# Kernel optimization log

Hardware: AMD Instinct MI355X
Metric: run time of the kernel (lower is better)

The kernel has to match this reference:

```python
import jax, jax.numpy as jnp
import numpy as np

STATE_LEN, SEQ_LEN, HIDDEN = 2048, 4096, 2048

def setup_inputs() -> dict:
    key = jax.random.key(0)
    k1, k2, k3, k4 = jax.random.split(key, 4)
    scale = 1.0 / np.sqrt(HIDDEN)
    return {
        "out_state": jax.random.normal(k1, (STATE_LEN, HIDDEN), dtype=jnp.float32),
        "history": jax.random.normal(k2, (SEQ_LEN, HIDDEN), dtype=jnp.float32),
        "W": jax.random.normal(k3, (HIDDEN, HIDDEN), dtype=jnp.float32) * scale,
        "b": jax.random.normal(k4, (HIDDEN,), dtype=jnp.float32) * scale,
    }

def reference(out_state, history, W, b):
    # method='general': energy_j = Linear(history_j) = history_j @ W.T + b
    # score[i, j] = out_state_i . energy_j  -> batched GEMM replacing the double loop
    energies = history @ W.T + b                 # [seq_len, hidden]
    scores = jnp.einsum('ih,jh->ij', out_state, energies)  # [state_len, seq_len]
    # F.softmax on a 2D tensor (legacy default) normalizes over dim=1 (rows)
    return jax.nn.softmax(scores, axis=-1)
```

## Files before the change

kernel.cpp:

```cpp
#include <hip/hip_runtime.h>


#define STATE_LEN 2048
#define SEQ_LEN   4096
#define HIDDEN    2048

#define BM 128
#define BK 32

typedef __bf16 bf16x8 __attribute__((ext_vector_type(8)));
typedef float f32x4 __attribute__((ext_vector_type(4)));

__device__ __forceinline__ unsigned short f32_to_bf16(float f) {
  unsigned u = __float_as_uint(f);
  u += 0x7FFFu + ((u >> 16) & 1u);
  return (unsigned short)(u >> 16);
}
__device__ __forceinline__ float bf16_to_f32(unsigned short h) {
  return __uint_as_float(((unsigned)h) << 16);
}

__device__ __forceinline__ void gld16(const void* g, void* l) {
  __builtin_amdgcn_global_load_lds(
      (const __attribute__((address_space(1))) unsigned int*)g,
      (__attribute__((address_space(3))) unsigned int*)l,
      16, 0, 0);
}

__global__ __launch_bounds__(256) void split_kernel(
    const float* __restrict__ in, unsigned short* __restrict__ hi,
    unsigned short* __restrict__ lo, int n) {
  int i = (blockIdx.x * 256 + threadIdx.x) * 4;
  if (i >= n) return;
  float4 v = *(const float4*)&in[i];
  ushort4 h, l;
  h.x = f32_to_bf16(v.x); l.x = f32_to_bf16(v.x - bf16_to_f32(h.x));
  h.y = f32_to_bf16(v.y); l.y = f32_to_bf16(v.y - bf16_to_f32(h.y));
  h.z = f32_to_bf16(v.z); l.z = f32_to_bf16(v.z - bf16_to_f32(h.z));
  h.w = f32_to_bf16(v.w); l.w = f32_to_bf16(v.w - bf16_to_f32(h.w));
  *(ushort4*)&hi[i] = h;
  *(ushort4*)&lo[i] = l;
}

__global__ __launch_bounds__(256) void transpose_split_kernel(
    const float* __restrict__ in, unsigned short* __restrict__ hi,
    unsigned short* __restrict__ lo, int rows, int cols) {
  __shared__ float tile[32][33];
  const int bx = blockIdx.x * 32;
  const int by = blockIdx.y * 32;
  const int tx = threadIdx.x;
  const int ty = threadIdx.y;
#pragma unroll
  for (int i = 0; i < 32; i += 8)
    tile[ty + i][tx] = in[(size_t)(by + ty + i) * cols + (bx + tx)];
  __syncthreads();
#pragma unroll
  for (int i = 0; i < 32; i += 8) {
    float x = tile[tx][ty + i];
    unsigned short h = f32_to_bf16(x);
    unsigned short l = f32_to_bf16(x - bf16_to_f32(h));
    size_t o = (size_t)(bx + ty + i) * rows + (by + tx);
    hi[o] = h;
    lo[o] = l;
  }
}

__global__ __launch_bounds__(256) void reduce_split4(
    const float* __restrict__ p0, const float* __restrict__ p1,
    const float* __restrict__ p2, const float* __restrict__ p3,
    unsigned short* __restrict__ hi, unsigned short* __restrict__ lo, int n) {
  int i = (blockIdx.x * 256 + threadIdx.x) * 4;
  if (i >= n) return;
  float4 a = *(const float4*)&p0[i];
  float4 b = *(const float4*)&p1[i];
  float4 c = *(const float4*)&p2[i];
  float4 d = *(const float4*)&p3[i];
  a.x = (a.x + b.x) + (c.x + d.x);
  a.y = (a.y + b.y) + (c.y + d.y);
  a.z = (a.z + b.z) + (c.z + d.z);
  a.w = (a.w + b.w) + (c.w + d.w);
  ushort4 h, l;
  h.x = f32_to_bf16(a.x); l.x = f32_to_bf16(a.x - bf16_to_f32(h.x));
  h.y = f32_to_bf16(a.y); l.y = f32_to_bf16(a.y - bf16_to_f32(h.y));
  h.z = f32_to_bf16(a.z); l.z = f32_to_bf16(a.z - bf16_to_f32(h.z));
  h.w = f32_to_bf16(a.w); l.w = f32_to_bf16(a.w - bf16_to_f32(h.w));
  *(ushort4*)&hi[i] = h;
  *(ushort4*)&lo[i] = l;
}

template <int BN, int KSPLIT>
__global__ __launch_bounds__(256, 4) void gemm_bt_split(
    const unsigned short* __restrict__ Ahi, const unsigned short* __restrict__ Alo,
    const unsigned short* __restrict__ Bhi, const unsigned short* __restrict__ Blo,
    float* __restrict__ Cf0, float* __restrict__ Cf1,
    float* __restrict__ Cf2, float* __restrict__ Cf3, int M, int N, int K) {
  constexpr int NI = BN / 32;
  __shared__ __align__(16) unsigned short sAhi[BM * BK];
  __shared__ __align__(16) unsigned short sAlo[BM * BK];
  __shared__ __align__(16) unsigned short sBhi[BN * BK];
  __shared__ __align__(16) unsigned short sBlo[BN * BK];

  const int t = threadIdx.x;
  const int tileM = blockIdx.y * BM;
  const int tileN = blockIdx.x * BN;
  const int z = (KSPLIT > 1) ? blockIdx.z : 0;
  const int kBase = z * (K / KSPLIT);
  const int kEnd = kBase + K / KSPLIT;
  float* Cf = Cf0;
  if (KSPLIT > 1) {
    if (z == 1) Cf = Cf1;
    else if (z == 2) Cf = Cf2;
    else if (z == 3) Cf = Cf3;
  }
  const int rr = t >> 2;
  const int cc = t & 3;

  const int lane = t & 63;
  const int wave = t >> 6;
  const int wm = wave >> 1;
  const int wn = wave & 1;
  const int lr = lane & 15;
  const int kqc = lane >> 4;

  f32x4 acc[4][NI] = {};

  for (int k0 = kBase; k0 < kEnd; k0 += BK) {
#pragma unroll
    for (int it = 0; it < 2; ++it) {
      const int r = it * 64 + rr;
      const int q = cc ^ ((r >> 1) & 3);
      const size_t ga = (size_t)(tileM + r) * K + k0 + q * 8;
      const int ls = r * BK + cc * 8;
      gld16(Ahi + ga, &sAhi[ls]);
      gld16(Alo + ga, &sAlo[ls]);
    }
#pragma unroll
    for (int it = 0; it < BN / 64; ++it) {
      const int r = it * 64 + rr;
      const int q = cc ^ ((r >> 1) & 3);
      const size_t gb = (size_t)(tileN + r) * K + k0 + q * 8;
      const int ls = r * BK + cc * 8;
      gld16(Bhi + gb, &sBhi[ls]);
      gld16(Blo + gb, &sBlo[ls]);
    }
    __syncthreads();

    bf16x8 ah[4], al[4], bh[NI], bl[NI];
#pragma unroll
    for (int mi = 0; mi < 4; ++mi) {
      const int R = wm * 64 + mi * 16 + lr;
      const int off = R * BK + (kqc ^ ((R >> 1) & 3)) * 8;
      ah[mi] = *(const bf16x8*)&sAhi[off];
      al[mi] = *(const bf16x8*)&sAlo[off];
    }
#pragma unroll
    for (int ni = 0; ni < NI; ++ni) {
      const int R = wn * (BN / 2) + ni * 16 + lr;
      const int off = R * BK + (kqc ^ ((R >> 1) & 3)) * 8;
      bh[ni] = *(const bf16x8*)&sBhi[off];
      bl[ni] = *(const bf16x8*)&sBlo[off];
    }
#pragma unroll
    for (int mi = 0; mi < 4; ++mi)
#pragma unroll
      for (int ni = 0; ni < NI; ++ni) {
        acc[mi][ni] = __builtin_amdgcn_mfma_f32_16x16x32_bf16(ah[mi], bh[ni], acc[mi][ni], 0, 0, 0);
        acc[mi][ni] = __builtin_amdgcn_mfma_f32_16x16x32_bf16(ah[mi], bl[ni], acc[mi][ni], 0, 0, 0);
        acc[mi][ni] = __builtin_amdgcn_mfma_f32_16x16x32_bf16(al[mi], bh[ni], acc[mi][ni], 0, 0, 0);
      }
    __syncthreads();
  }

#pragma unroll
  for (int mi = 0; mi < 4; ++mi)
#pragma unroll
    for (int ni = 0; ni < NI; ++ni)
#pragma unroll
      for (int e = 0; e < 4; ++e) {
        const int row = tileM + wm * 64 + mi * 16 + (lane >> 4) * 4 + e;
        const int col = tileN + wn * (BN / 2) + ni * 16 + lr;
        Cf[(size_t)row * N + col] = acc[mi][ni][e];
      }
}

__global__ __launch_bounds__(256) void reduce_softmax(float* __restrict__ d,
                                                      const float* __restrict__ part,
                                                      int cols) {
  const int row = blockIdx.x;
  float* p = d + (size_t)row * cols;
  const float* q = part + (size_t)row * cols;
  const int t = threadIdx.x;
  const int lane = t & 63;
  const int wave = t >> 6;
  __shared__ float sred[4];

  float4 v[4];
  float m = -3.0e38f;
#pragma unroll
  for (int k = 0; k < 4; ++k) {
    float4 a = *(const float4*)&p[(t + k * 256) * 4];
    float4 b = *(const float4*)&q[(t + k * 256) * 4];
    a.x += b.x; a.y += b.y; a.z += b.z; a.w += b.w;
    v[k] = a;
    m = fmaxf(m, fmaxf(fmaxf(a.x, a.y), fmaxf(a.z, a.w)));
  }
#pragma unroll
  for (int off = 32; off > 0; off >>= 1) m = fmaxf(m, __shfl_xor(m, off, 64));
  if (lane == 0) sred[wave] = m;
  __syncthreads();
  m = fmaxf(fmaxf(sred[0], sred[1]), fmaxf(sred[2], sred[3]));
  __syncthreads();

  float s = 0.f;
#pragma unroll
  for (int k = 0; k < 4; ++k) {
    v[k].x = __expf(v[k].x - m);
    v[k].y = __expf(v[k].y - m);
    v[k].z = __expf(v[k].z - m);
    v[k].w = __expf(v[k].w - m);
    s += (v[k].x + v[k].y) + (v[k].z + v[k].w);
  }
#pragma unroll
  for (int off = 32; off > 0; off >>= 1) s += __shfl_xor(s, off, 64);
  if (lane == 0) sred[wave] = s;
  __syncthreads();
  s = (sred[0] + sred[1]) + (sred[2] + sred[3]);
  const float inv = 1.0f / s;
#pragma unroll
  for (int k = 0; k < 4; ++k) {
    v[k].x *= inv; v[k].y *= inv; v[k].z *= inv; v[k].w *= inv;
    *(float4*)&p[(t + k * 256) * 4] = v[k];
  }
}

extern "C" void kernel_launch(void* const* d_in, const int* in_sizes, int n_in,
                              void* d_out, int out_size, void* d_ws, size_t ws_size,
                              hipStream_t stream) {
  const float* out_state = (const float*)d_in[0];
  const float* history   = (const float*)d_in[1];
  const float* W         = (const float*)d_in[2];
  float* out = (float*)d_out;

  char* ws = (char*)d_ws;
  const size_t MB = 1ull << 20;
  unsigned short* ohi  = (unsigned short*)(ws + 0 * MB);
  unsigned short* olo  = (unsigned short*)(ws + 8 * MB);
  unsigned short* wthi = (unsigned short*)(ws + 16 * MB);
  unsigned short* wtlo = (unsigned short*)(ws + 24 * MB);
  unsigned short* hhi  = (unsigned short*)(ws + 32 * MB);
  unsigned short* hlo  = (unsigned short*)(ws + 48 * MB);
  float*          pws  = (float*)(ws + 64 * MB);
  float* g1p0 = pws;
  float* g1p1 = pws + (size_t)STATE_LEN * HIDDEN;
  float* g1p2 = out;
  float* g1p3 = out + (size_t)STATE_LEN * HIDDEN;
  unsigned short* thi = (unsigned short*)(ws + 0 * MB);
  unsigned short* tlo = (unsigned short*)(ws + 8 * MB);

  split_kernel<<<(STATE_LEN * HIDDEN) / 1024, 256, 0, stream>>>(out_state, ohi, olo,
                                                                STATE_LEN * HIDDEN);
  transpose_split_kernel<<<dim3(HIDDEN / 32, HIDDEN / 32), dim3(32, 8), 0, stream>>>(
      W, wthi, wtlo, HIDDEN, HIDDEN);
  split_kernel<<<(SEQ_LEN * HIDDEN) / 1024, 256, 0, stream>>>(history, hhi, hlo,
                                                              SEQ_LEN * HIDDEN);
  gemm_bt_split<128, 4>
      <<<dim3(HIDDEN / 128, STATE_LEN / 128, 4), 256, 0, stream>>>(
          ohi, olo, wthi, wtlo, g1p0, g1p1, g1p2, g1p3, STATE_LEN, HIDDEN, HIDDEN);
  reduce_split4<<<(STATE_LEN * HIDDEN) / 1024, 256, 0, stream>>>(
      g1p0, g1p1, g1p2, g1p3, thi, tlo, STATE_LEN * HIDDEN);
  gemm_bt_split<128, 2>
      <<<dim3(SEQ_LEN / 128, STATE_LEN / 128, 2), 256, 0, stream>>>(
          thi, tlo, hhi, hlo, out, pws, nullptr, nullptr, STATE_LEN, SEQ_LEN, HIDDEN);
  reduce_softmax<<<STATE_LEN, 256, 0, stream>>>(out, pws, SEQ_LEN);
}
```

Before: 298.4 us.

## Load GEMM operands directly from global memory into registers, dropping LDS staging

The split-bf16 GEMM no longer stages A and B tiles through shared memory with global_load_lds and barriers. Each wave now reads its MFMA fragments straight from global memory into registers, which removes LDS traffic and the two __syncthreads per K step. The cost is that tile data is no longer shared between waves, so each operand fragment is fetched twice from global/L2. The 16-byte per-lane loads are also less coalesced, and launch bounds drop to 2 blocks per CU.

```diff
diff --git a/kernel.cpp b/kernel.cpp
--- a/kernel.cpp
+++ b/kernel.cpp
@@ -4,9 +4,6 @@
 #define STATE_LEN 2048
 #define SEQ_LEN   4096
 #define HIDDEN    2048
-
-#define BM 128
-#define BK 32
 
 typedef __bf16 bf16x8 __attribute__((ext_vector_type(8)));
 typedef float f32x4 __attribute__((ext_vector_type(4)));
@@ -18,13 +15,6 @@
 }
 __device__ __forceinline__ float bf16_to_f32(unsigned short h) {
   return __uint_as_float(((unsigned)h) << 16);
-}
-
-__device__ __forceinline__ void gld16(const void* g, void* l) {
-  __builtin_amdgcn_global_load_lds(
-      (const __attribute__((address_space(1))) unsigned int*)g,
-      (__attribute__((address_space(3))) unsigned int*)l,
-      16, 0, 0);
 }
 
 __global__ __launch_bounds__(256) void split_kernel(
@@ -88,32 +78,24 @@
   *(ushort4*)&lo[i] = l;
 }
 
-template <int BN, int KSPLIT>
-__global__ __launch_bounds__(256, 4) void gemm_bt_split(
+template <int KSPLIT>
+__global__ __launch_bounds__(256, 2) void gemm_direct(
     const unsigned short* __restrict__ Ahi, const unsigned short* __restrict__ Alo,
     const unsigned short* __restrict__ Bhi, const unsigned short* __restrict__ Blo,
     float* __restrict__ Cf0, float* __restrict__ Cf1,
     float* __restrict__ Cf2, float* __restrict__ Cf3, int M, int N, int K) {
-  constexpr int NI = BN / 32;
-  __shared__ __align__(16) unsigned short sAhi[BM * BK];
-  __shared__ __align__(16) unsigned short sAlo[BM * BK];
-  __shared__ __align__(16) unsigned short sBhi[BN * BK];
-  __shared__ __align__(16) unsigned short sBlo[BN * BK];
-
   const int t = threadIdx.x;
-  const int tileM = blockIdx.y * BM;
-  const int tileN = blockIdx.x * BN;
+  const int tileM = blockIdx.y * 128;
+  const int tileN = blockIdx.x * 128;
   const int z = (KSPLIT > 1) ? blockIdx.z : 0;
   const int kBase = z * (K / KSPLIT);
-  const int kEnd = kBase + K / KSPLIT;
+  const int iters = (K / KSPLIT) / 32;
   float* Cf = Cf0;
   if (KSPLIT > 1) {
     if (z == 1) Cf = Cf1;
     else if (z == 2) Cf = Cf2;
     else if (z == 3) Cf = Cf3;
   }
-  const int rr = t >> 2;
-  const int cc = t & 3;
 
   const int lane = t & 63;
   const int wave = t >> 6;
@@ -122,63 +104,47 @@
   const int lr = lane & 15;
   const int kqc = lane >> 4;
 
-  f32x4 acc[4][NI] = {};
-
-  for (int k0 = kBase; k0 < kEnd; k0 += BK) {
-#pragma unroll
-    for (int it = 0; it < 2; ++it) {
-      const int r = it * 64 + rr;
-      const int q = cc ^ ((r >> 1) & 3);
-      const size_t ga = (size_t)(tileM + r) * K + k0 + q * 8;
-      const int ls = r * BK + cc * 8;
-      gld16(Ahi + ga, &sAhi[ls]);
-      gld16(Alo + ga, &sAlo[ls]);
+  const size_t aRow = (size_t)(tileM + wm * 64 + lr) * K + kBase + kqc * 8;
+  const size_t bRow = (size_t)(tileN + wn * 64 + lr) * K + kBase + kqc * 8;
+  const unsigned short* pAh = Ahi + aRow;
+  const unsigned short* pAl = Alo + aRow;
+  const unsigned short* pBh = Bhi + bRow;
+  const unsigned short* pBl = Blo + bRow;
+  const size_t rstep = (size_t)16 * K;
+
+  f32x4 acc[4][4] = {};
+
+  for (int it = 0; it < iters; ++it) {
+    bf16x8 ah[4], al[4], bh[4], bl[4];
+#pragma unroll
+    for (int mi = 0; mi < 4; ++mi) {
+      ah[mi] = *(const bf16x8*)(pAh + mi * rstep);
+      al[mi] = *(const bf16x8*)(pAl + mi * rstep);
     }
 #pragma unroll
-    for (int it = 0; it < BN / 64; ++it) {
-      const int r = it * 64 + rr;
-      const int q = cc ^ ((r >> 1) & 3);
-      const size_t gb = (size_t)(tileN + r) * K + k0 + q * 8;
-      const int ls = r * BK + cc * 8;
-      gld16(Bhi + gb, &sBhi[ls]);
-      gld16(Blo + gb, &sBlo[ls]);
+    for (int ni = 0; ni < 4; ++ni) {
+      bh[ni] = *(const bf16x8*)(pBh + ni * rstep);
+      bl[ni] = *(const bf16x8*)(pBl + ni * rstep);
     }
-    __syncthreads();
-
-    bf16x8 ah[4], al[4], bh[NI], bl[NI];
-#pragma unroll
-    for (int mi = 0; mi < 4; ++mi) {
-      const int R = wm * 64 + mi * 16 + lr;
-      const int off = R * BK + (kqc ^ ((R >> 1) & 3)) * 8;
-      ah[mi] = *(const bf16x8*)&sAhi[off];
-      al[mi] = *(const bf16x8*)&sAlo[off];
-    }
-#pragma unroll
-    for (int ni = 0; ni < NI; ++ni) {
-      const int R = wn * (BN / 2) + ni * 16 + lr;
-      const int off = R * BK + (kqc ^ ((R >> 1) & 3)) * 8;
-      bh[ni] = *(const bf16x8*)&sBhi[off];
-      bl[ni] = *(const bf16x8*)&sBlo[off];
-    }
 #pragma unroll
     for (int mi = 0; mi < 4; ++mi)
 #pragma unroll
-      for (int ni = 0; ni < NI; ++ni) {
+      for (int ni = 0; ni < 4; ++ni) {
         acc[mi][ni] = __builtin_amdgcn_mfma_f32_16x16x32_bf16(ah[mi], bh[ni], acc[mi][ni], 0, 0, 0);
         acc[mi][ni] = __builtin_amdgcn_mfma_f32_16x16x32_bf16(ah[mi], bl[ni], acc[mi][ni], 0, 0, 0);
         acc[mi][ni] = __builtin_amdgcn_mfma_f32_16x16x32_bf16(al[mi], bh[ni], acc[mi][ni], 0, 0, 0);
       }
-    __syncthreads();
+    pAh += 32; pAl += 32; pBh += 32; pBl += 32;
   }
 
 #pragma unroll
   for (int mi = 0; mi < 4; ++mi)
 #pragma unroll
-    for (int ni = 0; ni < NI; ++ni)
+    for (int ni = 0; ni < 4; ++ni)
 #pragma unroll
       for (int e = 0; e < 4; ++e) {
         const int row = tileM + wm * 64 + mi * 16 + (lane >> 4) * 4 + e;
-        const int col = tileN + wn * (BN / 2) + ni * 16 + lr;
+        const int col = tileN + wn * 64 + ni * 16 + lr;
         Cf[(size_t)row * N + col] = acc[mi][ni][e];
       }
 }
@@ -263,12 +229,12 @@
       W, wthi, wtlo, HIDDEN, HIDDEN);
   split_kernel<<<(SEQ_LEN * HIDDEN) / 1024, 256, 0, stream>>>(history, hhi, hlo,
                                                               SEQ_LEN * HIDDEN);
-  gemm_bt_split<128, 4>
+  gemm_direct<4>
       <<<dim3(HIDDEN / 128, STATE_LEN / 128, 4), 256, 0, stream>>>(
           ohi, olo, wthi, wtlo, g1p0, g1p1, g1p2, g1p3, STATE_LEN, HIDDEN, HIDDEN);
   reduce_split4<<<(STATE_LEN * HIDDEN) / 1024, 256, 0, stream>>>(
       g1p0, g1p1, g1p2, g1p3, thi, tlo, STATE_LEN * HIDDEN);
-  gemm_bt_split<128, 2>
+  gemm_direct<2>
       <<<dim3(SEQ_LEN / 128, STATE_LEN / 128, 2), 256, 0, stream>>>(
           thi, tlo, hhi, hlo, out, pws, nullptr, nullptr, STATE_LEN, SEQ_LEN, HIDDEN);
   reduce_softmax<<<STATE_LEN, 256, 0, stream>>>(out, pws, SEQ_LEN);
```

Result: slower. 507.9 us (+70.2%).
